# Performance work log

Measured on AMD Instinct MI355X. Metric: run time of the kernel, lower is better.

## Reference

```python
import jax, jax.numpy as jnp
import numpy as np

TOKENS, IN_F, OUT_F = 8192, 4096, 4096

def setup_inputs() -> dict:
    key = jax.random.key(0)
    k1, k2, k3, k4 = jax.random.split(key, 4)
    # int8 activations and weights in [-127, 127]
    x = jax.random.randint(k1, (TOKENS, IN_F), -127, 128, dtype=jnp.int32).astype(jnp.int8)
    weight = jax.random.randint(k2, (OUT_F, IN_F), -127, 128, dtype=jnp.int32).astype(jnp.int8)  # [out, in]
    # static per-output-channel dequant scale (fp16), small so fp16 output doesn't overflow
    dequant_scale = (jax.random.uniform(k3, (OUT_F,), dtype=jnp.float32) * 1e-3).astype(jnp.float16)
    bias = (jax.random.normal(k4, (OUT_F,), dtype=jnp.float32)).astype(jnp.float16)
    return {"x": x, "weight": weight, "dequant_scale": dequant_scale, "bias": bias}

def reference(x, weight, dequant_scale, bias):
    # int8 GEMM with int32 accumulation: [tokens, in] @ [in, out] -> [tokens, out]
    acc = jax.lax.dot_general(
        x, weight.T,
        dimension_numbers=(((1,), (0,)), ((), ())),
        preferred_element_type=jnp.int32,
    )
    # static per-output-channel dequant, cast to fp16, add fp16 bias
    out = (acc.astype(jnp.float32) * dequant_scale.astype(jnp.float32)[None, :]).astype(jnp.float16)
    out = out + bias[None, :]
    # module returns (output, output_bias)
    return (out, bias)
```

## Files before the change

kernel.cpp:

```cpp
#include <hip/hip_runtime.h>
#include <hip/hip_fp16.h>
#include <stdint.h>

typedef __attribute__((ext_vector_type(4))) int int32x4;

#define TOKENS 8192
#define IN_F   4096
#define OUT_F  4096
#define BM 256
#define BN 256
#define BK 128
#define NT (IN_F / BK)

__global__ __launch_bounds__(256)
void pack_kernel(const int* __restrict__ src, uint32_t* __restrict__ dst, int n4)
{
    for (int i = blockIdx.x * 256 + threadIdx.x; i < n4; i += gridDim.x * 256) {
        int32x4 v = ((const int32x4*)src)[i];
        dst[i] = (uint32_t)(v[0] & 0xff) | ((uint32_t)(v[1] & 0xff) << 8) |
                 ((uint32_t)(v[2] & 0xff) << 16) | ((uint32_t)v[3] << 24);
    }
}

__global__ __launch_bounds__(512, 2)
void w8a8_gemm_kernel(const int8_t* __restrict__ x,
                      const int8_t* __restrict__ w,
                      const float* __restrict__ scale,
                      const float* __restrict__ bias,
                      float* __restrict__ out)
{
    __shared__ int8_t lA[2 * 2 * 128 * 128];
    __shared__ int8_t lB[2 * 2 * 128 * 128];

    const int tid = threadIdx.x;
    const int wv  = tid >> 6;
    const int l   = tid & 63;
    const int wqm = wv >> 1;
    const int wqn = wv & 1;

    const int bn = blockIdx.x;
    const int bm = blockIdx.y;

    const int8_t* baseA = x + (size_t)bm * BM * IN_F;
    const int8_t* baseB = w + (size_t)bn * BN * IN_F;

    const int seg0 = wv * 2, seg1 = wv * 2 + 1;
    const int r8   = l >> 3;
    const int swc  = (((l & 7) ^ r8) << 4);

    const int fr  = l & 15;
    const int xk  = (l & 7) << 4;
    const int cb0 = (l >> 4) << 4;

    int32x4 acc[2][2][2][4];
#pragma unroll
    for (int a0 = 0; a0 < 2; ++a0)
#pragma unroll
        for (int a1 = 0; a1 < 2; ++a1)
#pragma unroll
            for (int a2 = 0; a2 < 2; ++a2)
#pragma unroll
                for (int a3 = 0; a3 < 4; ++a3)
                    acc[a0][a1][a2][a3] = (int32x4){0, 0, 0, 0};

    int32x4 aF[2][2];
    int32x4 bF0[4][2];
    int32x4 bF1[4][2];

    auto stage_half = [&](int h4) {
        const int kt_ = h4 >> 2;
        const int wh_ = h4 & 3;
        const int8_t* sb = (wh_ < 2) ? baseA : baseB;
        int8_t* db = ((wh_ < 2) ? lA : lB) + ((kt_ & 1) << 15) + ((wh_ & 1) << 14);
        const size_t co = (size_t)kt_ * BK + swc;
        const size_t rb = (size_t)((wh_ & 1) * 128 + r8);
        __builtin_amdgcn_global_load_lds(
            (const __attribute__((address_space(1))) void*)(sb + (rb + seg0 * 8) * IN_F + co),
            (__attribute__((address_space(3))) void*)(db + seg0 * 1024), 16, 0, 0);
        __builtin_amdgcn_global_load_lds(
            (const __attribute__((address_space(1))) void*)(sb + (rb + seg1 * 8) * IN_F + co),
            (__attribute__((address_space(3))) void*)(db + seg1 * 1024), 16, 0, 0);
    };

#define LDA(MH)                                                                        \
    do {                                                                               \
        _Pragma("unroll") for (int mi = 0; mi < 2; ++mi)                               \
        _Pragma("unroll") for (int ks = 0; ks < 2; ++ks)                               \
            aF[mi][ks] = *(const int32x4*)&lAb[((MH) << 14) +                          \
                (wqm * 32 + mi * 16 + fr) * 128 + (((ks * 64) + cb0) ^ xk)];           \
    } while (0)

#define LDB(NH, DST)                                                                   \
    do {                                                                               \
        _Pragma("unroll") for (int ni = 0; ni < 4; ++ni)                               \
        _Pragma("unroll") for (int ks = 0; ks < 2; ++ks)                               \
            DST[ni][ks] = *(const int32x4*)&lBb[((NH) << 14) +                         \
                (wqn * 64 + ni * 16 + fr) * 128 + (((ks * 64) + cb0) ^ xk)];           \
    } while (0)

#define MMAQ(MH, NH, BF)                                                               \
    do {                                                                               \
        _Pragma("unroll") for (int mi = 0; mi < 2; ++mi)                               \
        _Pragma("unroll") for (int ni = 0; ni < 4; ++ni)                               \
        _Pragma("unroll") for (int ks = 0; ks < 2; ++ks)                               \
            acc[MH][NH][mi][ni] = __builtin_amdgcn_mfma_i32_16x16x64_i8(               \
                aF[mi][ks], BF[ni][ks], acc[MH][NH][mi][ni], 0, 0, 0);                 \
    } while (0)

#define PH(MH, NH, BF)                                                                 \
    do {                                                                               \
        __builtin_amdgcn_s_barrier();                                                  \
        asm volatile("s_waitcnt lgkmcnt(0)" ::: "memory");                             \
        __builtin_amdgcn_s_setprio(1);                                                 \
        MMAQ(MH, NH, BF);                                                              \
        __builtin_amdgcn_s_setprio(0);                                                 \
        __builtin_amdgcn_s_barrier();                                                  \
    } while (0)

    stage_half(0); stage_half(3); stage_half(1); stage_half(2);
    stage_half(4); stage_half(7);
    asm volatile("s_waitcnt vmcnt(4)" ::: "memory");
    __builtin_amdgcn_s_barrier();

    for (int t = 0; t < NT; ++t) {
        const int8_t* lAb = lA + ((t & 1) << 15);
        const int8_t* lBb = lB + ((t & 1) << 15);

        LDA(0); LDB(0, bF0);
        if (t + 1 < NT) stage_half(4 * (t + 1) + 1);
        PH(0, 0, bF0);

        LDB(1, bF1);
        if (t + 1 < NT) stage_half(4 * (t + 1) + 2);
        PH(0, 1, bF1);

        LDA(1);
        if (t + 2 < NT) stage_half(4 * (t + 2) + 0);
        PH(1, 1, bF1);

        if (t + 2 < NT) stage_half(4 * (t + 2) + 3);
        if (t + 2 < NT)      asm volatile("s_waitcnt vmcnt(4)" ::: "memory");
        else if (t + 1 < NT) asm volatile("s_waitcnt vmcnt(0)" ::: "memory");
        PH(1, 0, bF0);
    }

    const int r0 = (l >> 4) << 2;
#pragma unroll
    for (int NH = 0; NH < 2; ++NH)
#pragma unroll
        for (int ni = 0; ni < 4; ++ni) {
            const int col = bn * BN + NH * 128 + wqn * 64 + ni * 16 + fr;
            const float sc  = scale[col];
            const __half bs = __float2half(bias[col]);
#pragma unroll
            for (int MH = 0; MH < 2; ++MH)
#pragma unroll
                for (int mi = 0; mi < 2; ++mi) {
                    const int rowb = bm * BM + MH * 128 + wqm * 32 + mi * 16 + r0;
#pragma unroll
                    for (int r = 0; r < 4; ++r) {
                        __half h = __float2half((float)acc[MH][NH][mi][ni][r] * sc);
                        out[(size_t)(rowb + r) * OUT_F + col] = __half2float(__hadd(h, bs));
                    }
                }
        }
#undef LDA
#undef LDB
#undef MMAQ
#undef PH
}

__global__ void bias_copy_kernel(const float* __restrict__ bias, float* __restrict__ dst)
{
    const int i = blockIdx.x * 256 + threadIdx.x;
    if (i < OUT_F) dst[i] = bias[i];
}

extern "C" void kernel_launch(void* const* d_in, const int* in_sizes, int n_in,
                              void* d_out, int out_size, void* d_ws, size_t ws_size,
                              hipStream_t stream)
{
    const int*   x32   = (const int*)d_in[0];
    const int*   w32   = (const int*)d_in[1];
    const float* scale = (const float*)d_in[2];
    const float* bias  = (const float*)d_in[3];
    float* out = (float*)d_out;

    int8_t* x8 = (int8_t*)d_ws;
    int8_t* w8 = x8 + (size_t)TOKENS * IN_F;

    pack_kernel<<<2048, 256, 0, stream>>>(x32, (uint32_t*)x8, TOKENS * IN_F / 4);
    pack_kernel<<<2048, 256, 0, stream>>>(w32, (uint32_t*)w8, OUT_F * IN_F / 4);

    dim3 grid(OUT_F / BN, TOKENS / BM);
    w8a8_gemm_kernel<<<grid, 512, 0, stream>>>(x8, w8, scale, bias, out);
    bias_copy_kernel<<<OUT_F / 256, 256, 0, stream>>>(bias, out + (size_t)TOKENS * OUT_F);
}
```

Baseline: 211.6 us.

## Stage GEMM epilogue through LDS for coalesced stores and merge pack/bias kernels

The epilogue now writes int32 accumulators into shared memory in four 64-row chunks, using a padded stride. Threads then read them back as contiguous 4-column vectors and issue 16-byte coalesced float4 global stores, replacing the scattered 4-byte strided stores. The two pack launches and the bias copy launch are merged into one kernel to cut launch overhead. In exchange, the epilogue gains extra syncthreads barriers and LDS traffic, and the shared buffer becomes one unified 128KB array.

```diff
diff --git a/kernel.cpp b/kernel.cpp
--- a/kernel.cpp
+++ b/kernel.cpp
@@ -3,6 +3,7 @@
 #include <stdint.h>
 
 typedef __attribute__((ext_vector_type(4))) int int32x4;
+typedef __attribute__((ext_vector_type(4))) float float32x4;
 
 #define TOKENS 8192
 #define IN_F   4096
@@ -11,14 +12,27 @@
 #define BN 256
 #define BK 128
 #define NT (IN_F / BK)
+#define ESTR 260
 
 __global__ __launch_bounds__(256)
-void pack_kernel(const int* __restrict__ src, uint32_t* __restrict__ dst, int n4)
+void pack_all_kernel(const int* __restrict__ x32, const int* __restrict__ w32,
+                     const float* __restrict__ bias,
+                     uint32_t* __restrict__ x8, uint32_t* __restrict__ w8,
+                     float* __restrict__ bias_out)
 {
-    for (int i = blockIdx.x * 256 + threadIdx.x; i < n4; i += gridDim.x * 256) {
-        int32x4 v = ((const int32x4*)src)[i];
-        dst[i] = (uint32_t)(v[0] & 0xff) | ((uint32_t)(v[1] & 0xff) << 8) |
-                 ((uint32_t)(v[2] & 0xff) << 16) | ((uint32_t)v[3] << 24);
+    const int gid = blockIdx.x * 256 + threadIdx.x;
+    if (gid < OUT_F / 4)
+        ((float32x4*)bias_out)[gid] = ((const float32x4*)bias)[gid];
+
+    const int nx4 = TOKENS * IN_F / 4;
+    const int nw4 = OUT_F * IN_F / 4;
+    for (int i = gid; i < nx4 + nw4; i += gridDim.x * 256) {
+        const int* s; uint32_t* d; int j;
+        if (i < nx4) { s = x32; d = x8; j = i; }
+        else         { s = w32; d = w8; j = i - nx4; }
+        int32x4 v = ((const int32x4*)s)[j];
+        d[j] = (uint32_t)(v[0] & 0xff) | ((uint32_t)(v[1] & 0xff) << 8) |
+               ((uint32_t)(v[2] & 0xff) << 16) | ((uint32_t)v[3] << 24);
     }
 }
 
@@ -29,8 +43,9 @@
                       const float* __restrict__ bias,
                       float* __restrict__ out)
 {
-    __shared__ int8_t lA[2 * 2 * 128 * 128];
-    __shared__ int8_t lB[2 * 2 * 128 * 128];
+    __shared__ int8_t smem[131072];
+    int8_t* lA = smem;
+    int8_t* lB = smem + 65536;
 
     const int tid = threadIdx.x;
     const int wv  = tid >> 6;
@@ -144,36 +159,51 @@
         PH(1, 0, bF0);
     }
 
+    __syncthreads();
+    int* eL = (int*)smem;
+    const int c4   = tid & 63;
+    const int rowt = tid >> 6;
+    const float32x4 sc4 = ((const float32x4*)scale)[bn * 64 + c4];
+    const float32x4 bf4 = ((const float32x4*)bias )[bn * 64 + c4];
+    const __half bh[4] = { __float2half(bf4[0]), __float2half(bf4[1]),
+                           __float2half(bf4[2]), __float2half(bf4[3]) };
     const int r0 = (l >> 4) << 2;
-#pragma unroll
-    for (int NH = 0; NH < 2; ++NH)
-#pragma unroll
-        for (int ni = 0; ni < 4; ++ni) {
-            const int col = bn * BN + NH * 128 + wqn * 64 + ni * 16 + fr;
-            const float sc  = scale[col];
-            const __half bs = __float2half(bias[col]);
-#pragma unroll
-            for (int MH = 0; MH < 2; ++MH)
-#pragma unroll
-                for (int mi = 0; mi < 2; ++mi) {
-                    const int rowb = bm * BM + MH * 128 + wqm * 32 + mi * 16 + r0;
-#pragma unroll
-                    for (int r = 0; r < 4; ++r) {
-                        __half h = __float2half((float)acc[MH][NH][mi][ni][r] * sc);
-                        out[(size_t)(rowb + r) * OUT_F + col] = __half2float(__hadd(h, bs));
-                    }
-                }
+    const int wr0 = (wqm & 1) * 32 + r0;
+
+    for (int c = 0; c < 4; ++c) {
+        if ((wqm >> 1) == (c & 1)) {
+            const int MH = c >> 1;
+#pragma unroll
+            for (int NH = 0; NH < 2; ++NH)
+#pragma unroll
+                for (int mi = 0; mi < 2; ++mi)
+#pragma unroll
+                    for (int ni = 0; ni < 4; ++ni)
+#pragma unroll
+                        for (int r = 0; r < 4; ++r)
+                            eL[(wr0 + mi * 16 + r) * ESTR +
+                               NH * 128 + wqn * 64 + ni * 16 + fr] = acc[MH][NH][mi][ni][r];
         }
+        __syncthreads();
+#pragma unroll
+        for (int p = 0; p < 8; ++p) {
+            const int rl = p * 8 + rowt;
+            int32x4 v = *(const int32x4*)&eL[rl * ESTR + c4 * 4];
+            float32x4 o;
+#pragma unroll
+            for (int j = 0; j < 4; ++j) {
+                __half h = __float2half((float)v[j] * sc4[j]);
+                o[j] = __half2float(__hadd(h, bh[j]));
+            }
+            const size_t rowg = (size_t)(bm * 256 + c * 64 + rl);
+            ((float32x4*)out)[rowg * (OUT_F / 4) + bn * 64 + c4] = o;
+        }
+        __syncthreads();
+    }
 #undef LDA
 #undef LDB
 #undef MMAQ
 #undef PH
-}
-
-__global__ void bias_copy_kernel(const float* __restrict__ bias, float* __restrict__ dst)
-{
-    const int i = blockIdx.x * 256 + threadIdx.x;
-    if (i < OUT_F) dst[i] = bias[i];
 }
 
 extern "C" void kernel_launch(void* const* d_in, const int* in_sizes, int n_in,
@@ -189,10 +219,9 @@
     int8_t* x8 = (int8_t*)d_ws;
     int8_t* w8 = x8 + (size_t)TOKENS * IN_F;
 
-    pack_kernel<<<2048, 256, 0, stream>>>(x32, (uint32_t*)x8, TOKENS * IN_F / 4);
-    pack_kernel<<<2048, 256, 0, stream>>>(w32, (uint32_t*)w8, OUT_F * IN_F / 4);
+    pack_all_kernel<<<3072, 256, 0, stream>>>(x32, w32, bias, (uint32_t*)x8, (uint32_t*)w8,
+                                              out + (size_t)TOKENS * OUT_F);
 
     dim3 grid(OUT_F / BN, TOKENS / BM);
     w8a8_gemm_kernel<<<grid, 512, 0, stream>>>(x8, w8, scale, bias, out);
-    bias_copy_kernel<<<OUT_F / 256, 256, 0, stream>>>(bias, out + (size_t)TOKENS * OUT_F);
 }
```

Result: faster. 196.3 us (-7.2%).
